# Optimization experiments

Hardware: AMD Instinct MI355X
Metric: run time of the kernel (lower is better)

The kernel has to match this reference:

```python
import jax, jax.numpy as jnp
import numpy as np

L, B, I, H = 256, 16, 2048, 2048
S = R = T = 32  # s_size == t_size is required by the read-hop chaining


def setup_inputs() -> dict:
    key = jax.random.key(0)
    ks = jax.random.split(key, 8)
    def p(k, shape, scale=0.02):
        return jax.random.normal(k, shape, jnp.float32) * scale
    return dict(
        inputs=jax.random.normal(ks[0], (L, B, I), jnp.float32),
        h0=jnp.zeros((B, H), jnp.float32),
        c0=jnp.zeros((B, H), jnp.float32),
        F0=jnp.zeros((B, S * R, T), jnp.float32),
        W_ih=p(ks[1], (4 * H, I)),
        W_hh=p(ks[2], (4 * H, H)),
        b_ih=jnp.zeros((4 * H,), jnp.float32),
        b_hh=jnp.zeros((4 * H,), jnp.float32),
        Ww_w=p(ks[3], (S + R + T + 1, H)),
        Ww_b=jnp.zeros((S + R + T + 1,), jnp.float32),
        Wr_w=p(ks[4], (S + 3 * R, H)),
        Wr_b=jnp.zeros((S + 3 * R,), jnp.float32),
        Wlin_w=p(ks[5], (H, T)),
        Wlin_b=jnp.zeros((H,), jnp.float32),
    )


def _ln(x, eps=1e-5):
    # LayerNorm without affine params (elementwise_affine=False)
    m = jnp.mean(x, -1, keepdims=True)
    v = jnp.var(x, -1, keepdims=True)
    return (x - m) * jax.lax.rsqrt(v + eps)


def reference(inputs, h0, c0, F0, W_ih, W_hh, b_ih, b_hh,
              Ww_w, Ww_b, Wr_w, Wr_b, Wlin_w, Wlin_b):
    # ---- single-layer LSTM (PyTorch gate order i,f,g,o) ----
    bias = b_ih + b_hh
    def lstm_step(carry, x_t):
        h, c = carry
        g = x_t @ W_ih.T + h @ W_hh.T + bias            # [B,4H]
        i, f, gg, o = jnp.split(g, 4, axis=-1)
        c = jax.nn.sigmoid(f) * c + jax.nn.sigmoid(i) * jnp.tanh(gg)
        h = jax.nn.sigmoid(o) * jnp.tanh(c)
        return (h, c), h
    _, x = jax.lax.scan(lstm_step, (h0, c0), inputs)     # x: [L,B,H]

    # ---- Fast Weight Memory: per-step write then 3-hop read ----
    def fwm_step(Fm, x_t):
        # write
        w = x_t @ Ww_w.T + Ww_b                          # [B, S+R+T+1]
        s = jnp.tanh(w[:, :S])
        r = jnp.tanh(w[:, S:S + R])
        t = jnp.tanh(w[:, S + R:S + R + T])
        b = jax.nn.sigmoid(w[:, S + R + T:] + 1.0)       # [B,1]
        sr = (s[:, :, None] * r[:, None, :]).reshape(-1, S * R)   # [B,S*R]
        v = jnp.einsum('bk,bkt->bt', sr, Fm)             # [B,T]
        Fm = Fm + sr[:, :, None] * (b * (t - v))[:, None, :]
        n = jnp.linalg.norm(Fm.reshape(Fm.shape[0], -1), axis=-1)
        Fm = Fm / (jax.nn.relu(n - 1.0) + 1.0)[:, None, None]
        # read (3 hops)
        rv = jnp.tanh(x_t @ Wr_w.T + Wr_b)               # [B, S+3R]
        q = rv[:, :S]
        for j in range(3):
            rj = rv[:, S + j * R:S + (j + 1) * R]
            nr = (q[:, :, None] * rj[:, None, :]).reshape(q.shape[0], -1)
            q = _ln(jnp.einsum('bk,bkt->bt', nr, Fm))    # [B,T]
        return Fm, q

    _, qs = jax.lax.scan(fwm_step, F0, x)                # qs: [L,B,T]
    return x + qs @ Wlin_w.T + Wlin_b                    # [L,B,H]
```

## Files before the change

kernel.cpp:

```cpp
#include <hip/hip_runtime.h>
#include <hip/hip_bf16.h>
#include <cstdint>
#include <cstddef>

#define L_DIM 256
#define B_DIM 16
#define I_DIM 2048
#define H_DIM 2048
#define G4    8192
#define MROWS 4096
#define NWGL  128
#define NPRJ  16
#define NSCN  16

typedef __hip_bfloat16 bf16;
typedef __bf16 bf16x8_t __attribute__((ext_vector_type(8)));
typedef _Float16 f16x8_t __attribute__((ext_vector_type(8)));
typedef float f32x4_t   __attribute__((ext_vector_type(4)));

__device__ __forceinline__ bf16 f2b(float f) { return __float2bfloat16(f); }

__device__ __forceinline__ void gl_lds16(const void* g, void* l) {
  __builtin_amdgcn_global_load_lds(
      (const __attribute__((address_space(1))) unsigned int*)g,
      (__attribute__((address_space(3))) unsigned int*)l, 16, 0, 0);
}

__device__ __forceinline__ float sigmoidf_(float x) { return 1.f / (1.f + expf(-x)); }

__device__ __forceinline__ f16x8_t load_f16x8_sc(const _Float16* p) {
  f16x8_t r;
  asm volatile("global_load_dwordx4 %0, %1, off sc0 sc1" : "=v"(r) : "v"(p));
  return r;
}
__device__ __forceinline__ bf16x8_t load_bf16x8_sc(const bf16* p) {
  bf16x8_t r;
  asm volatile("global_load_dwordx4 %0, %1, off sc0 sc1" : "=v"(r) : "v"(p));
  return r;
}
__device__ __forceinline__ float load_f32_sc(const float* p) {
  float r;
  asm volatile("global_load_dword %0, %1, off sc0 sc1" : "=v"(r) : "v"(p));
  return r;
}
__device__ __forceinline__ void store_short_sc(void* p, unsigned int v) {
  asm volatile("global_store_short %0, %1, off sc0 sc1" :: "v"(p), "v"(v) : "memory");
}
__device__ __forceinline__ void store_f32_sc(void* p, float v) {
  asm volatile("global_store_dword %0, %1, off sc0 sc1" :: "v"(p), "v"(v) : "memory");
}

__global__ void prep_kernel(const float* __restrict__ Wih, const float* __restrict__ Whh,
                            const float* __restrict__ inp, const float* __restrict__ Www,
                            const float* __restrict__ Wwb, const float* __restrict__ Wrw,
                            const float* __restrict__ h0,
                            _Float16* __restrict__ Wih_f, _Float16* __restrict__ Whh_f,
                            _Float16* __restrict__ inp_f,
                            bf16* __restrict__ Wq_hi, bf16* __restrict__ Wq_lo,
                            bf16* __restrict__ Wr_hi, bf16* __restrict__ Wr_lo,
                            float* __restrict__ wbpad,
                            _Float16* __restrict__ Xh0)
{
  size_t idx0 = (size_t)blockIdx.x * blockDim.x + threadIdx.x;
  size_t stride = (size_t)gridDim.x * blockDim.x;
  for (size_t i = idx0; i < 16777216ull; i += stride) {
    Wih_f[i] = (_Float16)Wih[i];
    Whh_f[i] = (_Float16)Whh[i];
  }
  for (size_t i = idx0; i < 8388608ull; i += stride) inp_f[i] = (_Float16)inp[i];
  for (size_t i = idx0; i < 262144ull; i += stride) {
    size_t r = i >> 11;
    float q = (r < 97) ? Www[i] : 0.f;
    bf16 qh = f2b(q);
    Wq_hi[i] = qh;
    Wq_lo[i] = f2b(q - (float)qh);
    float rr = Wrw[i];
    bf16 rh = f2b(rr);
    Wr_hi[i] = rh;
    Wr_lo[i] = f2b(rr - (float)rh);
  }
  for (size_t i = idx0; i < 128ull; i += stride) wbpad[i] = (i < 97) ? Wwb[i] : 0.f;
  for (size_t i = idx0; i < 32768ull; i += stride) Xh0[i] = (_Float16)h0[i];
}

__global__ __launch_bounds__(256) void gemm_f16(const _Float16* __restrict__ A,
                                                const _Float16* __restrict__ B,
                                                const float* __restrict__ bih,
                                                const float* __restrict__ bhh,
                                                _Float16* __restrict__ Gin2,
                                                int M, int N, int K)
{
  __shared__ __align__(16) _Float16 As[128 * 32];
  __shared__ __align__(16) _Float16 Bs[128 * 32];
  const int tid  = threadIdx.x;
  const int lane = tid & 63;
  const int w    = tid >> 6;
  const int wm   = w >> 1, wn = w & 1;
  const int m0   = blockIdx.x * 128, n0 = blockIdx.y * 128;

  f32x4_t acc[4][4];
#pragma unroll
  for (int m = 0; m < 4; ++m)
#pragma unroll
    for (int n = 0; n < 4; ++n) acc[m][n] = (f32x4_t){0.f, 0.f, 0.f, 0.f};

  for (int k0 = 0; k0 < K; k0 += 32) {
#pragma unroll
    for (int r = 0; r < 2; ++r) {
      const int base = w * 2048 + r * 1024;
      const int off  = base + lane * 16;
      const int e    = off >> 1;
      const int row  = e >> 5;
      const int col  = e & 31;
      gl_lds16(A + (size_t)(m0 + row) * K + (k0 + col), (char*)As + base);
      gl_lds16(B + (size_t)(n0 + row) * K + (k0 + col), (char*)Bs + base);
    }
    __syncthreads();

    f16x8_t af[4], bfr[4];
    const int kb = (lane >> 4) * 16;
#pragma unroll
    for (int m = 0; m < 4; ++m)
      af[m] = *reinterpret_cast<const f16x8_t*>((const char*)As + (wm * 64 + m * 16 + (lane & 15)) * 64 + kb);
#pragma unroll
    for (int n = 0; n < 4; ++n)
      bfr[n] = *reinterpret_cast<const f16x8_t*>((const char*)Bs + (wn * 64 + n * 16 + (lane & 15)) * 64 + kb);
#pragma unroll
    for (int m = 0; m < 4; ++m)
#pragma unroll
      for (int n = 0; n < 4; ++n)
        acc[m][n] = __builtin_amdgcn_mfma_f32_16x16x32_f16(af[m], bfr[n], acc[m][n], 0, 0, 0);
    __syncthreads();
  }

#pragma unroll
  for (int m = 0; m < 4; ++m) {
#pragma unroll
    for (int n = 0; n < 4; ++n) {
      const int col  = n0 + wn * 64 + n * 16 + (lane & 15);
      const float bv = bih[col] + bhh[col];
      const int gate = col >> 11, j = col & 2047;
      const int wg = j >> 4, jj = j & 15;
#pragma unroll
      for (int r = 0; r < 4; ++r) {
        const int row = m0 + wm * 64 + m * 16 + (lane >> 4) * 4 + r;
        const int t = row >> 4, bb = row & 15;
        const size_t idx = ((((size_t)t * NWGL + wg) * 4 + gate) * 16 + jj) * 16 + bb;
        Gin2[idx] = (_Float16)(acc[m][n][r] + bv);
      }
    }
  }
}

__global__ __launch_bounds__(512, 2) void fused_rnn(
    const _Float16* __restrict__ Whh,
    const _Float16* __restrict__ Gin2,
    const float* __restrict__ bih, const float* __restrict__ bhh,
    const float* __restrict__ c0,
    const bf16* __restrict__ Wq_hi, const bf16* __restrict__ Wq_lo,
    const bf16* __restrict__ Wr_hi, const bf16* __restrict__ Wr_lo,
    const float* __restrict__ wbpad, const float* __restrict__ Wrb,
    const float* __restrict__ F0,
    _Float16* __restrict__ Xh,
    bf16* __restrict__ XhHi, bf16* __restrict__ XhLo,
    float* __restrict__ Wall, float* __restrict__ RVall,
    float* __restrict__ Gbuf,
    int* lflags, int* pflags)
{
  __shared__ float part[8][4][16][17];
  __shared__ float s_s[32], s_r[32], s_tv[32], s_bb;
  __shared__ float s_rv[128];
  __shared__ float s_v[32];
  __shared__ float s_red[8];

  const int wgid = blockIdx.x;
  const int tid  = threadIdx.x;
  const int lane = tid & 63;
  const int wv   = tid >> 6;

  if (wgid < NWGL) {
    const int wg = wgid;
    const int j0 = wg * 16;
    const int kw = wv * 256;

    f16x8_t whh[4][8];
    {
      const int nn  = lane & 15;
      const int kfo = (lane >> 4) * 8;
#pragma unroll
      for (int g = 0; g < 4; ++g) {
        const size_t grow = (size_t)(g * H_DIM + j0 + nn) * 2048;
#pragma unroll
        for (int ks = 0; ks < 8; ++ks)
          whh[g][ks] = *reinterpret_cast<const f16x8_t*>(Whh + grow + kw + ks * 32 + kfo);
      }
    }

    float c_reg = 0.f, cbr0 = 0.f, cbr1 = 0.f, cbr2 = 0.f, cbr3 = 0.f;
    if (tid < 256) {
      const int bb = tid & 15, jj = tid >> 4;
      const int j = j0 + jj;
      c_reg = c0[bb * H_DIM + j];
      cbr0 = bih[0 * H_DIM + j] + bhh[0 * H_DIM + j];
      cbr1 = bih[1 * H_DIM + j] + bhh[1 * H_DIM + j];
      cbr2 = bih[2 * H_DIM + j] + bhh[2 * H_DIM + j];
      cbr3 = bih[3 * H_DIM + j] + bhh[3 * H_DIM + j];
    }

    const size_t arow = (size_t)(lane & 15) * 2048 + kw + (lane >> 4) * 8;
    const int fidx = ((wv << 4) + (lane & 15)) << 4;

    for (int t = 0; t < L_DIM; ++t) {
      if (t > 0) {
        while (true) {
          const int v = __hip_atomic_load(&lflags[fidx], __ATOMIC_RELAXED,
                                          __HIP_MEMORY_SCOPE_AGENT);
          if (__all(v >= t)) break;
          __builtin_amdgcn_s_sleep(1);
        }
      }

      float gin0 = 0.f, gin1 = 0.f, gin2v = 0.f, gin3 = 0.f;
      if (tid < 256) {
        const _Float16* gbase = Gin2 + ((size_t)t * NWGL + wg) * 1024;
        gin0  = (float)gbase[0 * 256 + tid];
        gin1  = (float)gbase[1 * 256 + tid];
        gin2v = (float)gbase[2 * 256 + tid];
        gin3  = (float)gbase[3 * 256 + tid];
      }

      const size_t hoff = (size_t)t * 32768 + arow;
      f16x8_t hf[8];
#pragma unroll
      for (int ks = 0; ks < 8; ++ks)
        hf[ks] = load_f16x8_sc(Xh + hoff + ks * 32);
      asm volatile("s_waitcnt vmcnt(0)" ::: "memory");
      __builtin_amdgcn_sched_barrier(0);

      f32x4_t acc[4];
#pragma unroll
      for (int g = 0; g < 4; ++g) acc[g] = (f32x4_t){0.f, 0.f, 0.f, 0.f};
#pragma unroll
      for (int ks = 0; ks < 8; ++ks) {
#pragma unroll
        for (int g = 0; g < 4; ++g)
          acc[g] = __builtin_amdgcn_mfma_f32_16x16x32_f16(hf[ks], whh[g][ks], acc[g], 0, 0, 0);
      }
#pragma unroll
      for (int g = 0; g < 4; ++g)
#pragma unroll
        for (int r = 0; r < 4; ++r)
          part[wv][g][(lane >> 4) * 4 + r][lane & 15] = acc[g][r];
      __syncthreads();

      if (tid < 256) {
        const int bb = tid & 15, jj = tid >> 4;
        float g4[4] = {gin0, gin1, gin2v, gin3};
        const float cb4[4] = {cbr0, cbr1, cbr2, cbr3};
#pragma unroll
        for (int g = 0; g < 4; ++g) {
          float s = 0.f;
#pragma unroll
          for (int v = 0; v < 8; ++v) s += part[v][g][bb][jj];
          g4[g] += s + cb4[g];
        }
        const float i_ = sigmoidf_(g4[0]);
        const float f_ = sigmoidf_(g4[1]);
        const float g_ = tanhf(g4[2]);
        const float o_ = sigmoidf_(g4[3]);
        c_reg = f_ * c_reg + i_ * g_;
        const float h = o_ * tanhf(c_reg);
        const int bj = bb * 2048 + j0 + jj;
        const _Float16 hF = (_Float16)h;
        const bf16 hhv = f2b(h);
        const bf16 hlv = f2b(h - (float)hhv);
        const size_t xi = ((size_t)t * 16 + bb) * 2048 + j0 + jj;
        store_short_sc(Xh + (size_t)(t + 1) * 32768 + bj,
                       (unsigned int)__builtin_bit_cast(unsigned short, hF));
        store_short_sc(XhHi + xi,
                       (unsigned int)__builtin_bit_cast(unsigned short, hhv));
        store_short_sc(XhLo + xi,
                       (unsigned int)__builtin_bit_cast(unsigned short, hlv));
      }
      asm volatile("s_waitcnt vmcnt(0)" ::: "memory");
      __syncthreads();

      if (tid == 0)
        __hip_atomic_store(&lflags[wg << 4], t + 1, __ATOMIC_RELAXED,
                           __HIP_MEMORY_SCOPE_AGENT);
    }

  } else if (wgid < NWGL + NPRJ) {
    const int p   = wgid - NWGL;
    const int kw  = wv * 256;
    const int nn  = lane & 15;
    const int kfo = (lane >> 4) * 8;

    bf16x8_t wbh[8], wbl[8];
    {
      const bf16* Bh = (p < 8) ? Wq_hi : Wr_hi;
      const bf16* Bl = (p < 8) ? Wq_lo : Wr_lo;
      const int brow = (p < 8) ? (p * 16 + nn) : ((p - 8) * 16 + nn);
#pragma unroll
      for (int ks = 0; ks < 8; ++ks) {
        const size_t o = (size_t)brow * 2048 + kw + ks * 32 + kfo;
        wbh[ks] = *reinterpret_cast<const bf16x8_t*>(Bh + o);
        wbl[ks] = *reinterpret_cast<const bf16x8_t*>(Bl + o);
      }
    }
    float biasv = 0.f;
    if (tid < 256) {
      const int oo = tid >> 4;
      biasv = (p < 8) ? wbpad[p * 16 + oo] : Wrb[(p - 8) * 16 + oo];
    }

    const size_t axrow = (size_t)(lane & 15) * 2048 + kw + kfo;

    for (int t = 0; t < L_DIM; ++t) {
      while (true) {
        const int v0 = __hip_atomic_load(&lflags[lane << 4], __ATOMIC_RELAXED,
                                         __HIP_MEMORY_SCOPE_AGENT);
        const int v1 = __hip_atomic_load(&lflags[(64 + lane) << 4], __ATOMIC_RELAXED,
                                         __HIP_MEMORY_SCOPE_AGENT);
        if (__all(v0 > t && v1 > t)) break;
        __builtin_amdgcn_s_sleep(1);
      }

      const size_t xoff = (size_t)t * 32768 + axrow;
      bf16x8_t xh[8], xl[8];
#pragma unroll
      for (int ks = 0; ks < 8; ++ks) {
        xh[ks] = load_bf16x8_sc(XhHi + xoff + ks * 32);
        xl[ks] = load_bf16x8_sc(XhLo + xoff + ks * 32);
      }
      asm volatile("s_waitcnt vmcnt(0)" ::: "memory");
      __builtin_amdgcn_sched_barrier(0);

      f32x4_t acc = {0.f, 0.f, 0.f, 0.f};
#pragma unroll
      for (int ks = 0; ks < 8; ++ks) {
        acc = __builtin_amdgcn_mfma_f32_16x16x32_bf16(xh[ks], wbh[ks], acc, 0, 0, 0);
        acc = __builtin_amdgcn_mfma_f32_16x16x32_bf16(xh[ks], wbl[ks], acc, 0, 0, 0);
        acc = __builtin_amdgcn_mfma_f32_16x16x32_bf16(xl[ks], wbh[ks], acc, 0, 0, 0);
      }
#pragma unroll
      for (int r = 0; r < 4; ++r)
        part[wv][0][(lane >> 4) * 4 + r][lane & 15] = acc[r];
      __syncthreads();

      if (tid < 256) {
        const int bb = tid & 15, oo = tid >> 4;
        float s = 0.f;
#pragma unroll
        for (int v = 0; v < 8; ++v) s += part[v][0][bb][oo];
        s += biasv;
        float* dst;
        if (p < 8) {
          dst = Wall + (size_t)(t * 16 + bb) * 128 + p * 16 + oo;
        } else {
          s = tanhf(s);
          dst = RVall + (size_t)(t * 16 + bb) * 128 + (p - 8) * 16 + oo;
        }
        store_f32_sc(dst, s);
      }
      asm volatile("s_waitcnt vmcnt(0)" ::: "memory");
      __syncthreads();

      if (tid == 0)
        __hip_atomic_store(&pflags[p << 4], t + 1, __ATOMIC_RELAXED,
                           __HIP_MEMORY_SCOPE_AGENT);
    }

  } else {
    const int b     = wgid - NWGL - NPRJ;
    const int si    = lane >> 1;
    const int rbase = 16 * (lane & 1);
    const int tl    = lane & 31;

    float F[16][4];
#pragma unroll
    for (int i = 0; i < 16; ++i)
#pragma unroll
      for (int j = 0; j < 4; ++j)
        F[i][j] = F0[((size_t)b * 1024 + (16 * lane + i)) * 32 + 4 * wv + j];

    float N = 0.f;
    {
      float loc = 0.f;
#pragma unroll
      for (int i = 0; i < 16; ++i)
#pragma unroll
        for (int j = 0; j < 4; ++j) loc += F[i][j] * F[i][j];
#pragma unroll
      for (int m = 1; m < 64; m <<= 1) loc += __shfl_xor(loc, m);
      if (lane == 0) s_red[wv] = loc;
      __syncthreads();
#pragma unroll
      for (int k = 0; k < 8; ++k) N += s_red[k];
    }

    for (int t = 0; t < 256; ++t) {
      while (true) {
        const int v = __hip_atomic_load(&pflags[(lane & 15) << 4], __ATOMIC_RELAXED,
                                        __HIP_MEMORY_SCOPE_AGENT);
        if (__all(v > t)) break;
        __builtin_amdgcn_s_sleep(1);
      }

      float wpre = 0.f, rvpre = 0.f;
      if (tid < 97)  wpre = load_f32_sc(Wall + (size_t)(t * 16 + b) * 128 + tid);
      if (tid >= 128 && tid < 256)
        rvpre = load_f32_sc(RVall + (size_t)(t * 16 + b) * 128 + tid - 128);
      asm volatile("s_waitcnt vmcnt(0)" ::: "memory");
      __syncthreads();
      if (tid < 32)       s_s[tid]       = tanhf(wpre);
      else if (tid < 64)  s_r[tid - 32]  = tanhf(wpre);
      else if (tid < 96)  s_tv[tid - 64] = tanhf(wpre);
      else if (tid == 96) s_bb           = sigmoidf_(wpre + 1.f);
      else if (tid >= 128 && tid < 256) s_rv[tid - 128] = rvpre;
      __syncthreads();

      const float sv = s_s[si];
      float sr[16];
#pragma unroll
      for (int i = 0; i < 16; ++i) sr[i] = sv * s_r[rbase + i];

      float vv4[4];
#pragma unroll
      for (int j = 0; j < 4; ++j) {
        float pp = 0.f;
#pragma unroll
        for (int i = 0; i < 16; ++i) pp += sr[i] * F[i][j];
#pragma unroll
        for (int m = 1; m < 64; m <<= 1) pp += __shfl_xor(pp, m);
        vv4[j] = pp;
      }
      if (lane == 0) {
#pragma unroll
        for (int j = 0; j < 4; ++j) s_v[4 * wv + j] = vv4[j];
      }
      __syncthreads();

      const float vt  = s_v[tl];
      const float ut  = s_bb * (s_tv[tl] - vt);
      const float sl  = s_s[tl];
      const float rl  = s_r[tl];
      float uv = ut * vt, uu = ut * ut, ss = sl * sl, rr = rl * rl;
#pragma unroll
      for (int m = 1; m < 32; m <<= 1) {
        uv += __shfl_xor(uv, m);
        uu += __shfl_xor(uu, m);
        ss += __shfl_xor(ss, m);
        rr += __shfl_xor(rr, m);
      }
      const float Np  = N + 2.f * uv + ss * rr * uu;
      const float n_  = sqrtf(Np);
      const float inv = 1.f / (fmaxf(n_ - 1.f, 0.f) + 1.f);
      N = Np * inv * inv;

      float uw[4];
#pragma unroll
      for (int j = 0; j < 4; ++j) uw[j] = __shfl(ut, 4 * wv + j);
#pragma unroll
      for (int i = 0; i < 16; ++i)
#pragma unroll
        for (int j = 0; j < 4; ++j)
          F[i][j] = (F[i][j] + sr[i] * uw[j]) * inv;

      float* gout = Gbuf + ((size_t)(t * 16 + b) * 3) * 1024;
#pragma unroll
      for (int jit = 0; jit < 3; ++jit) {
        float rjv[16];
#pragma unroll
        for (int i = 0; i < 16; ++i) rjv[i] = s_rv[32 + 32 * jit + rbase + i];
        f32x4_t gv;
#pragma unroll
        for (int j = 0; j < 4; ++j) {
          float g = 0.f;
#pragma unroll
          for (int i = 0; i < 16; ++i) g += rjv[i] * F[i][j];
          g += __shfl_xor(g, 1);
          gv[j] = g;
        }
        if ((lane & 1) == 0)
          *reinterpret_cast<f32x4_t*>(gout + jit * 1024 + (lane >> 1) * 32 + 4 * wv) = gv;
      }
    }
  }
}

__global__ __launch_bounds__(256) void fwm_qread(const float* __restrict__ Gbuf,
                                                 const float* __restrict__ RVall,
                                                 float* __restrict__ QS)
{
  const int pair = blockIdx.x * 4 + (threadIdx.x >> 6);
  const int lane = threadIdx.x & 63;
  const int tq    = lane & 31;
  const int ihalf = (lane >> 5) * 16;

  const float* G  = Gbuf + (size_t)pair * 3 * 1024;
  float q = RVall[(size_t)pair * 128 + tq];
#pragma unroll 1
  for (int jit = 0; jit < 3; ++jit) {
    float c = 0.f;
#pragma unroll
    for (int i = 0; i < 16; ++i) {
      const float qi = __shfl(q, ihalf + i);
      c += qi * G[jit * 1024 + (ihalf + i) * 32 + tq];
    }
    c += __shfl_xor(c, 32);
    float mval = c;
#pragma unroll
    for (int m = 1; m < 32; m <<= 1) mval += __shfl_xor(mval, m);
    mval *= (1.f / 32.f);
    const float dl = c - mval;
    float var = dl * dl;
#pragma unroll
    for (int m = 1; m < 32; m <<= 1) var += __shfl_xor(var, m);
    var *= (1.f / 32.f);
    q = dl * rsqrtf(var + 1e-5f);
  }
  if (lane < 32) QS[(size_t)pair * 32 + lane] = q;
}

__global__ __launch_bounds__(256) void out_kernel(const bf16* __restrict__ Xh1Hi,
                                                  const bf16* __restrict__ Xh1Lo,
                                                  const float* __restrict__ QS,
                                                  const float* __restrict__ Wlin,
                                                  const float* __restrict__ blin,
                                                  float* __restrict__ out)
{
  __shared__ float qs[32];
  const int row = blockIdx.x;
  if (threadIdx.x < 32) qs[threadIdx.x] = QS[(size_t)row * 32 + threadIdx.x];
  __syncthreads();
  for (int h = threadIdx.x; h < H_DIM; h += 256) {
    const size_t xi = (size_t)row * H_DIM + h;
    float acc = (float)Xh1Hi[xi] + (float)Xh1Lo[xi] + blin[h];
    const float* wr = Wlin + (size_t)h * 32;
#pragma unroll
    for (int t2 = 0; t2 < 32; ++t2) acc += qs[t2] * wr[t2];
    out[xi] = acc;
  }
}

extern "C" void kernel_launch(void* const* d_in, const int* in_sizes, int n_in,
                              void* d_out, int out_size, void* d_ws, size_t ws_size,
                              hipStream_t stream)
{
  (void)in_sizes; (void)n_in; (void)out_size; (void)ws_size;
  const float* inp  = (const float*)d_in[0];
  const float* h0   = (const float*)d_in[1];
  const float* c0   = (const float*)d_in[2];
  const float* F0   = (const float*)d_in[3];
  const float* Wih  = (const float*)d_in[4];
  const float* Whh  = (const float*)d_in[5];
  const float* bih  = (const float*)d_in[6];
  const float* bhh  = (const float*)d_in[7];
  const float* Www  = (const float*)d_in[8];
  const float* Wwb  = (const float*)d_in[9];
  const float* Wrw  = (const float*)d_in[10];
  const float* Wrb  = (const float*)d_in[11];
  const float* Wlin = (const float*)d_in[12];
  const float* blin = (const float*)d_in[13];
  float* out = (float*)d_out;

  char* p = (char*)d_ws;
  auto alloc = [&](size_t bytes) {
    char* r = p;
    p += (bytes + 255) & ~(size_t)255;
    return r;
  };
  _Float16* Whh_f = (_Float16*)alloc(16777216ull * 2);
  _Float16* Wih_f = (_Float16*)alloc(16777216ull * 2);
  _Float16* inp_f = (_Float16*)alloc(8388608ull * 2);
  _Float16* Gin2  = (_Float16*)alloc(33554432ull * 2);
  _Float16* Xh    = (_Float16*)alloc(257ull * 32768 * 2);
  bf16*  Wq_hi  = (bf16*)alloc(262144ull * 2);
  bf16*  Wq_lo  = (bf16*)alloc(262144ull * 2);
  bf16*  Wr_hi  = (bf16*)alloc(262144ull * 2);
  bf16*  Wr_lo  = (bf16*)alloc(262144ull * 2);
  float* wbpad  = (float*)alloc(128ull * 4);
  float* Wall   = (float*)alloc(524288ull * 4);
  float* RVall  = (float*)alloc(524288ull * 4);
  float* QS     = (float*)alloc(131072ull * 4);
  float* Gbuf   = (float*)alloc(12582912ull * 4);
  int*   flags  = (int*)alloc((NWGL + NPRJ) * 64);
  int*   lflags = flags;
  int*   pflags = flags + NWGL * 16;
  bf16*  XhHi  = (bf16*)inp_f;
  bf16*  XhLo  = (bf16*)Wih_f;

  prep_kernel<<<2048, 256, 0, stream>>>(Wih, Whh, inp, Www, Wwb, Wrw, h0,
                                        Wih_f, Whh_f, inp_f,
                                        Wq_hi, Wq_lo, Wr_hi, Wr_lo, wbpad, Xh);

  gemm_f16<<<dim3(32, 64), 256, 0, stream>>>(inp_f, Wih_f, bih, bhh, Gin2,
                                             MROWS, G4, 2048);

  hipMemsetAsync(flags, 0, (NWGL + NPRJ) * 64, stream);
  {
    void* kargs[] = {
      (void*)&Whh_f, (void*)&Gin2, (void*)&bih, (void*)&bhh, (void*)&c0,
      (void*)&Wq_hi, (void*)&Wq_lo, (void*)&Wr_hi, (void*)&Wr_lo,
      (void*)&wbpad, (void*)&Wrb, (void*)&F0,
      (void*)&Xh, (void*)&XhHi, (void*)&XhLo,
      (void*)&Wall, (void*)&RVall, (void*)&Gbuf,
      (void*)&lflags, (void*)&pflags
    };
    hipLaunchCooperativeKernel((const void*)fused_rnn,
                               dim3(NWGL + NPRJ + NSCN), dim3(512),
                               kargs, 0, stream);
  }

  fwm_qread<<<1024, 256, 0, stream>>>(Gbuf, RVall, QS);

  out_kernel<<<4096, 256, 0, stream>>>(XhHi, XhLo, QS, Wlin, blin, out);
}
```

Baseline: 1.905 ms.

## Fuse FWM read hops into output kernel and store Gbuf as fp16

Merges the q-read kernel into the output kernel, so each block computes its own row's three read hops into shared memory before applying the output projection. This removes one launch and the QS round trip. The per-step Gbuf read matrices are now stored in fp16, halving their traffic, and the GEMM epilogue writes Gin2 as 4-wide fp16 vectors instead of scalar stores. It also gives XhLo its own buffer rather than aliasing Wih_f. The fp16 Gbuf loses precision ahead of the layer-norm hops, and only one wave per block does the hop work while the other three wait.

After: 1.873 ms. About the same (-1.7%).

```diff
diff --git a/kernel.cpp b/kernel.cpp
--- a/kernel.cpp
+++ b/kernel.cpp
@@ -16,6 +16,7 @@
 typedef __hip_bfloat16 bf16;
 typedef __bf16 bf16x8_t __attribute__((ext_vector_type(8)));
 typedef _Float16 f16x8_t __attribute__((ext_vector_type(8)));
+typedef _Float16 f16x4_t __attribute__((ext_vector_type(4)));
 typedef float f32x4_t   __attribute__((ext_vector_type(4)));
 
 __device__ __forceinline__ bf16 f2b(float f) { return __float2bfloat16(f); }
@@ -41,6 +42,11 @@
 __device__ __forceinline__ float load_f32_sc(const float* p) {
   float r;
   asm volatile("global_load_dword %0, %1, off sc0 sc1" : "=v"(r) : "v"(p));
+  return r;
+}
+__device__ __forceinline__ unsigned int load_u16_sc(const _Float16* p) {
+  unsigned int r;
+  asm volatile("global_load_ushort %0, %1, off sc0 sc1" : "=v"(r) : "v"(p));
   return r;
 }
 __device__ __forceinline__ void store_short_sc(void* p, unsigned int v) {
@@ -133,21 +139,22 @@
     __syncthreads();
   }
 
-#pragma unroll
-  for (int m = 0; m < 4; ++m) {
-#pragma unroll
-    for (int n = 0; n < 4; ++n) {
-      const int col  = n0 + wn * 64 + n * 16 + (lane & 15);
-      const float bv = bih[col] + bhh[col];
-      const int gate = col >> 11, j = col & 2047;
-      const int wg = j >> 4, jj = j & 15;
-#pragma unroll
-      for (int r = 0; r < 4; ++r) {
-        const int row = m0 + wm * 64 + m * 16 + (lane >> 4) * 4 + r;
-        const int t = row >> 4, bb = row & 15;
-        const size_t idx = ((((size_t)t * NWGL + wg) * 4 + gate) * 16 + jj) * 16 + bb;
-        Gin2[idx] = (_Float16)(acc[m][n][r] + bv);
-      }
+  const int jj = lane & 15;
+#pragma unroll
+  for (int n = 0; n < 4; ++n) {
+    const int colb = n0 + wn * 64 + n * 16;
+    const int gate = colb >> 11;
+    const int wg   = (colb & 2047) >> 4;
+    const float bv = bih[colb + jj] + bhh[colb + jj];
+#pragma unroll
+    for (int m = 0; m < 4; ++m) {
+      const int rowb = m0 + wm * 64 + m * 16;
+      const int t = rowb >> 4;
+      f16x4_t v4;
+#pragma unroll
+      for (int r = 0; r < 4; ++r) v4[r] = (_Float16)(acc[m][n][r] + bv);
+      *reinterpret_cast<f16x4_t*>(
+          Gin2 + (((size_t)t * NWGL + wg) * 4 + gate) * 256 + jj * 16 + (lane >> 4) * 4) = v4;
     }
   }
 }
@@ -164,7 +171,7 @@
     _Float16* __restrict__ Xh,
     bf16* __restrict__ XhHi, bf16* __restrict__ XhLo,
     float* __restrict__ Wall, float* __restrict__ RVall,
-    float* __restrict__ Gbuf,
+    _Float16* __restrict__ Gbuf,
     int* lflags, int* pflags)
 {
   __shared__ float part[8][4][16][17];
@@ -467,74 +474,71 @@
         for (int j = 0; j < 4; ++j)
           F[i][j] = (F[i][j] + sr[i] * uw[j]) * inv;
 
-      float* gout = Gbuf + ((size_t)(t * 16 + b) * 3) * 1024;
+      _Float16* gout = Gbuf + ((size_t)(t * 16 + b) * 3) * 1024;
 #pragma unroll
       for (int jit = 0; jit < 3; ++jit) {
         float rjv[16];
 #pragma unroll
         for (int i = 0; i < 16; ++i) rjv[i] = s_rv[32 + 32 * jit + rbase + i];
-        f32x4_t gv;
+        f16x4_t gv;
 #pragma unroll
         for (int j = 0; j < 4; ++j) {
           float g = 0.f;
 #pragma unroll
           for (int i = 0; i < 16; ++i) g += rjv[i] * F[i][j];
           g += __shfl_xor(g, 1);
-          gv[j] = g;
+          gv[j] = (_Float16)g;
         }
         if ((lane & 1) == 0)
-          *reinterpret_cast<f32x4_t*>(gout + jit * 1024 + (lane >> 1) * 32 + 4 * wv) = gv;
-      }
-    }
-  }
-}
-
-__global__ __launch_bounds__(256) void fwm_qread(const float* __restrict__ Gbuf,
+          *reinterpret_cast<f16x4_t*>(gout + jit * 1024 + (lane >> 1) * 32 + 4 * wv) = gv;
+      }
+    }
+  }
+}
+
+__global__ __launch_bounds__(256) void qread_out(const _Float16* __restrict__ Gbuf,
                                                  const float* __restrict__ RVall,
-                                                 float* __restrict__ QS)
-{
-  const int pair = blockIdx.x * 4 + (threadIdx.x >> 6);
-  const int lane = threadIdx.x & 63;
-  const int tq    = lane & 31;
-  const int ihalf = (lane >> 5) * 16;
-
-  const float* G  = Gbuf + (size_t)pair * 3 * 1024;
-  float q = RVall[(size_t)pair * 128 + tq];
-#pragma unroll 1
-  for (int jit = 0; jit < 3; ++jit) {
-    float c = 0.f;
-#pragma unroll
-    for (int i = 0; i < 16; ++i) {
-      const float qi = __shfl(q, ihalf + i);
-      c += qi * G[jit * 1024 + (ihalf + i) * 32 + tq];
-    }
-    c += __shfl_xor(c, 32);
-    float mval = c;
-#pragma unroll
-    for (int m = 1; m < 32; m <<= 1) mval += __shfl_xor(mval, m);
-    mval *= (1.f / 32.f);
-    const float dl = c - mval;
-    float var = dl * dl;
-#pragma unroll
-    for (int m = 1; m < 32; m <<= 1) var += __shfl_xor(var, m);
-    var *= (1.f / 32.f);
-    q = dl * rsqrtf(var + 1e-5f);
-  }
-  if (lane < 32) QS[(size_t)pair * 32 + lane] = q;
-}
-
-__global__ __launch_bounds__(256) void out_kernel(const bf16* __restrict__ Xh1Hi,
-                                                  const bf16* __restrict__ Xh1Lo,
-                                                  const float* __restrict__ QS,
-                                                  const float* __restrict__ Wlin,
-                                                  const float* __restrict__ blin,
-                                                  float* __restrict__ out)
+                                                 const bf16* __restrict__ Xh1Hi,
+                                                 const bf16* __restrict__ Xh1Lo,
+                                                 const float* __restrict__ Wlin,
+                                                 const float* __restrict__ blin,
+                                                 float* __restrict__ out)
 {
   __shared__ float qs[32];
   const int row = blockIdx.x;
-  if (threadIdx.x < 32) qs[threadIdx.x] = QS[(size_t)row * 32 + threadIdx.x];
+  const int tid = threadIdx.x;
+
+  if (tid < 64) {
+    const int lane  = tid;
+    const int tq    = lane & 31;
+    const int ihalf = (lane >> 5) * 16;
+    const _Float16* G = Gbuf + (size_t)row * 3 * 1024;
+    float q = RVall[(size_t)row * 128 + tq];
+#pragma unroll 1
+    for (int jit = 0; jit < 3; ++jit) {
+      float c = 0.f;
+#pragma unroll
+      for (int i = 0; i < 16; ++i) {
+        const float qi = __shfl(q, ihalf + i);
+        c += qi * (float)G[jit * 1024 + (ihalf + i) * 32 + tq];
+      }
+      c += __shfl_xor(c, 32);
+      float mval = c;
+#pragma unroll
+      for (int m = 1; m < 32; m <<= 1) mval += __shfl_xor(mval, m);
+      mval *= (1.f / 32.f);
+      const float dl = c - mval;
+      float var = dl * dl;
+#pragma unroll
+      for (int m = 1; m < 32; m <<= 1) var += __shfl_xor(var, m);
+      var *= (1.f / 32.f);
+      q = dl * rsqrtf(var + 1e-5f);
+    }
+    if (lane < 32) qs[lane] = q;
+  }
   __syncthreads();
-  for (int h = threadIdx.x; h < H_DIM; h += 256) {
+
+  for (int h = tid; h < H_DIM; h += 256) {
     const size_t xi = (size_t)row * H_DIM + h;
     float acc = (float)Xh1Hi[xi] + (float)Xh1Lo[xi] + blin[h];
     const float* wr = Wlin + (size_t)h * 32;
@@ -576,6 +580,7 @@
   _Float16* inp_f = (_Float16*)alloc(8388608ull * 2);
   _Float16* Gin2  = (_Float16*)alloc(33554432ull * 2);
   _Float16* Xh    = (_Float16*)alloc(257ull * 32768 * 2);
+  bf16*     XhLo  = (bf16*)alloc(8388608ull * 2);
   bf16*  Wq_hi  = (bf16*)alloc(262144ull * 2);
   bf16*  Wq_lo  = (bf16*)alloc(262144ull * 2);
   bf16*  Wr_hi  = (bf16*)alloc(262144ull * 2);
@@ -583,13 +588,11 @@
   float* wbpad  = (float*)alloc(128ull * 4);
   float* Wall   = (float*)alloc(524288ull * 4);
   float* RVall  = (float*)alloc(524288ull * 4);
-  float* QS     = (float*)alloc(131072ull * 4);
-  float* Gbuf   = (float*)alloc(12582912ull * 4);
+  _Float16* Gbuf = (_Float16*)alloc(12582912ull * 2);
   int*   flags  = (int*)alloc((NWGL + NPRJ) * 64);
   int*   lflags = flags;
   int*   pflags = flags + NWGL * 16;
   bf16*  XhHi  = (bf16*)inp_f;
-  bf16*  XhLo  = (bf16*)Wih_f;
 
   prep_kernel<<<2048, 256, 0, stream>>>(Wih, Whh, inp, Www, Wwb, Wrw, h0,
                                         Wih_f, Whh_f, inp_f,
@@ -613,7 +616,5 @@
                                kargs, 0, stream);
   }
 
-  fwm_qread<<<1024, 256, 0, stream>>>(Gbuf, RVall, QS);
-
-  out_kernel<<<4096, 256, 0, stream>>>(XhHi, XhLo, QS, Wlin, blin, out);
-}
+  qread_out<<<4096, 256, 0, stream>>>(Gbuf, RVall, XhHi, XhLo, Wlin, blin, out);
+}
```
